# Performance work log

Measured on AMD Instinct MI355X. Metric: run time of the kernel, lower is better.

## Reference

```python
import jax, jax.numpy as jnp
from jax import lax
import numpy as np

L, T, B, F, H = 2, 512, 128, 4, 256


def _qweight(r, i, j, k):
    # Parcollet quaternion linear: W [in, out] from components [in//4, out//4]
    cr = jnp.concatenate([r, -i, -j, -k], axis=0)
    ci = jnp.concatenate([i, r, -k, j], axis=0)
    cj = jnp.concatenate([j, k, r, -i], axis=0)
    ck = jnp.concatenate([k, -j, i, r], axis=0)
    return jnp.concatenate([cr, ci, cj, ck], axis=1)


def _qlstm_layer(x, wr, wi, wj, wk, wb, ur, ui, uj, uk, fw, fb):
    # x: [T, B, F_in]; gate order (f, i, o, c) along axis 0 of the stacked params
    Wx = jax.vmap(_qweight)(wr, wi, wj, wk)          # [4, F_in, H]
    Uh = jax.vmap(_qweight)(ur, ui, uj, uk)          # [4, H, H]
    g = jnp.einsum('tbf,gfh->tgbh', x, Wx) + wb[None, :, None, :]  # [T,4,B,H]
    h0 = jnp.zeros((x.shape[1], Uh.shape[-1]), x.dtype)

    def step(carry, gt):
        h, c = carry
        pre = gt + jnp.einsum('bh,ghk->gbk', h, Uh)   # [4,B,H]
        ft = jax.nn.sigmoid(pre[0])
        it = jax.nn.sigmoid(pre[1])
        ot = jax.nn.sigmoid(pre[2])
        c = it * jnp.tanh(pre[3]) + ft * c
        h = ot * jnp.tanh(c)
        return (h, c), h @ fw + fb

    _, out = lax.scan(step, (h0, h0), g)              # [T, B, F_out]
    norm = jnp.linalg.norm(out, axis=2, keepdims=True)
    return out / jnp.maximum(norm, 1e-12)


def setup_inputs() -> dict:
    key = jax.random.key(0)
    ks = jax.random.split(key, 12)
    s = 0.05
    return {
        'x': jax.random.normal(ks[0], (B, T, F), jnp.float32),
        'Wx_r': jax.random.normal(ks[1], (L, 4, F // 4, H // 4), jnp.float32) * s,
        'Wx_i': jax.random.normal(ks[2], (L, 4, F // 4, H // 4), jnp.float32) * s,
        'Wx_j': jax.random.normal(ks[3], (L, 4, F // 4, H // 4), jnp.float32) * s,
        'Wx_k': jax.random.normal(ks[4], (L, 4, F // 4, H // 4), jnp.float32) * s,
        'Wx_b': jax.random.normal(ks[5], (L, 4, H), jnp.float32) * s,
        'Uh_r': jax.random.normal(ks[6], (L, 4, H // 4, H // 4), jnp.float32) * s,
        'Uh_i': jax.random.normal(ks[7], (L, 4, H // 4, H // 4), jnp.float32) * s,
        'Uh_j': jax.random.normal(ks[8], (L, 4, H // 4, H // 4), jnp.float32) * s,
        'Uh_k': jax.random.normal(ks[9], (L, 4, H // 4, H // 4), jnp.float32) * s,
        'fco_w': jax.random.normal(ks[10], (L, H, F), jnp.float32) * s,
        'fco_b': jax.random.normal(ks[11], (L, F), jnp.float32) * s,
    }


def reference(x, Wx_r, Wx_i, Wx_j, Wx_k, Wx_b, Uh_r, Uh_i, Uh_j, Uh_k, fco_w, fco_b):
    h = jnp.transpose(x, (1, 0, 2))  # batch_first -> [T, B, F]
    for l in range(L):
        h = _qlstm_layer(h, Wx_r[l], Wx_i[l], Wx_j[l], Wx_k[l], Wx_b[l],
                         Uh_r[l], Uh_i[l], Uh_j[l], Uh_k[l], fco_w[l], fco_b[l])
    h = jnp.transpose(h, (1, 0, 2))  # back to [B, T, F]
    return h[:, -1, :]
```

## Files before the change

kernel.cpp:

```cpp
#include <hip/hip_runtime.h>

#define L_ 2
#define T_ 512
#define B_ 128
#define F_ 4
#define H_ 256
#define QSIGN_MASK 0x5390
#define LOG2E  1.4426950408889634f
#define LOG2E2 2.8853900817779268f

typedef __attribute__((ext_vector_type(8))) short short8;
typedef __attribute__((ext_vector_type(4))) float f32x4;

__device__ unsigned long long g_inter_q[T_][B_];

__global__ void zero_inter() {
  ((unsigned long long*)g_inter_q)[blockIdx.x * 256 + threadIdx.x] = 0ull;
}

__device__ __forceinline__ unsigned f2bf(float f) {
  unsigned u = __float_as_uint(f);
  return (u + 0x7fff + ((u >> 16) & 1)) >> 16;
}
__device__ __forceinline__ float sig2(float y) {
  return __builtin_amdgcn_rcpf(1.f + __builtin_amdgcn_exp2f(-y));
}
__device__ __forceinline__ float tanh2(float y) {
  return fmaf(2.f, __builtin_amdgcn_rcpf(1.f + __builtin_amdgcn_exp2f(-y)), -1.f);
}
__device__ __forceinline__ unsigned long long pack4bf(float a, float b, float c, float d) {
  unsigned lo, hi;
  asm("v_cvt_pk_bf16_f32 %0, %1, %2" : "=v"(lo) : "v"(a), "v"(b));
  asm("v_cvt_pk_bf16_f32 %0, %1, %2" : "=v"(hi) : "v"(c), "v"(d));
  return ((unsigned long long)hi << 32) | lo;
}

union FragU { short8 v; uint4 u; unsigned w[4]; };

__launch_bounds__(320, 1)
__global__ void qlstm_fused(const float* __restrict__ x_in,
                            const float* __restrict__ uhr, const float* __restrict__ uhi,
                            const float* __restrict__ uhj, const float* __restrict__ uhk,
                            const float* __restrict__ wxr, const float* __restrict__ wxi,
                            const float* __restrict__ wxj, const float* __restrict__ wxk,
                            const float* __restrict__ wxb_all,
                            const float* __restrict__ fcw_all, const float* __restrict__ fcb_all,
                            float* __restrict__ out_final)
{
  __shared__ __align__(16) unsigned short sh_h[2][4][272];
  __shared__ unsigned long long sh_x[4][4];

  const int t     = threadIdx.x;
  const int role  = blockIdx.x >> 5;
  const int bg    = blockIdx.x & 31;
  const int bg0   = bg * 4;
  const int layer = role;
  const int wv    = t >> 6;
  const int lane  = t & 63;
  const int quad  = lane >> 4;
  const int sub   = lane & 15;

  const float* wb = wxb_all + layer * 4 * H_;
  const float* fw = fcw_all + layer * H_ * F_;
  const float* fb = fcb_all + layer * F_;

  for (int i = t; i < 2176; i += 320) ((unsigned short*)sh_h)[i] = 0;

  if (wv < 4) {
    const int u  = wv * 16 + sub;
    const int ba = sub >> 2;
    const int qa = sub & 3;

    FragU Bf[32];
    FragU Bx[4];
    f32x4 bvv[4];
    {
      const float* Cc[4] = {uhr, uhi, uhj, uhk};
      const float* Xc[4] = {wxr, wxi, wxj, wxk};
      #pragma unroll
      for (int g = 0; g < 4; ++g) {
        const float kg = (g == 3) ? LOG2E2 : LOG2E;
        #pragma unroll
        for (int ks = 0; ks < 8; ++ks) {
          const int d  = ks >> 1;
          const int pp = (ks & 1) * 32 + quad * 8;
          const float* src = Cc[d] + (size_t)((layer * 4 + g) * 64 + pp) * 64 + u;
          FragU f;
          #pragma unroll
          for (int j = 0; j < 8; ++j) f.v[j] = (short)f2bf(src[j * 64] * kg);
          Bf[g * 8 + ks] = f;
        }
        FragU fx; fx.w[0] = 0; fx.w[1] = 0; fx.w[2] = 0; fx.w[3] = 0;
        if (quad == 0) {
          unsigned e0 = f2bf(Xc[0][(layer * 4 + g) * 64 + u] * kg);
          unsigned e1 = f2bf(Xc[1][(layer * 4 + g) * 64 + u] * kg);
          unsigned e2 = f2bf(Xc[2][(layer * 4 + g) * 64 + u] * kg);
          unsigned e3 = f2bf(Xc[3][(layer * 4 + g) * 64 + u] * kg);
          fx.w[0] = e0 | (e1 << 16);
          fx.w[1] = e2 | (e3 << 16);
        }
        Bx[g] = fx;
        f32x4 bv;
        #pragma unroll
        for (int r = 0; r < 4; ++r) bv[r] = wb[g * 256 + r * 64 + u] * kg;
        bvv[g] = bv;
      }
    }
    unsigned smask[4], smx[4];
    int xsh[4], aoff[8];
    #pragma unroll
    for (int d = 0; d < 4; ++d) {
      const int a = qa ^ d;
      const bool neg = (QSIGN_MASK >> (a * 4 + qa)) & 1;
      smask[d] = neg ? 0x80008000u : 0u;
      smx[d]   = neg ? 0x8000u : 0u;
      xsh[d]   = 16 * a;
    }
    #pragma unroll
    for (int ks = 0; ks < 8; ++ks)
      aoff[ks] = ba * 544 + (((qa ^ (ks >> 1)) * 64 + (ks & 1) * 32 + quad * 8) << 1);
    float cs[4] = {0.f, 0.f, 0.f, 0.f};
    __syncthreads();

    const char* hbB = (const char*)sh_h;
    for (int s = 0; s <= T_; ++s) {
      if (s < T_) {
        const char* hp = hbB + ((s + 1) & 1) * 2176;
        unsigned long long xq = sh_x[s & 3][ba];
        FragU Ax; Ax.w[0] = 0; Ax.w[1] = 0; Ax.w[2] = 0; Ax.w[3] = 0;
        if (quad == 0) {
          unsigned e0 = ((unsigned)(xq >> xsh[0]) & 0xffffu) ^ smx[0];
          unsigned e1 = ((unsigned)(xq >> xsh[1]) & 0xffffu) ^ smx[1];
          unsigned e2 = ((unsigned)(xq >> xsh[2]) & 0xffffu) ^ smx[2];
          unsigned e3 = ((unsigned)(xq >> xsh[3]) & 0xffffu) ^ smx[3];
          Ax.w[0] = e0 | (e1 << 16);
          Ax.w[1] = e2 | (e3 << 16);
        }
        f32x4 acc0 = __builtin_amdgcn_mfma_f32_16x16x32_bf16(Ax.v, Bx[0].v, bvv[0], 0, 0, 0);
        f32x4 acc1 = __builtin_amdgcn_mfma_f32_16x16x32_bf16(Ax.v, Bx[1].v, bvv[1], 0, 0, 0);
        f32x4 acc2 = __builtin_amdgcn_mfma_f32_16x16x32_bf16(Ax.v, Bx[2].v, bvv[2], 0, 0, 0);
        f32x4 acc3 = __builtin_amdgcn_mfma_f32_16x16x32_bf16(Ax.v, Bx[3].v, bvv[3], 0, 0, 0);
        #pragma unroll
        for (int ks = 0; ks < 8; ++ks) {
          FragU A;
          A.u = *(const uint4*)(hp + aoff[ks]);
          const unsigned m = smask[ks >> 1];
          A.w[0] ^= m; A.w[1] ^= m; A.w[2] ^= m; A.w[3] ^= m;
          acc0 = __builtin_amdgcn_mfma_f32_16x16x32_bf16(A.v, Bf[0 * 8 + ks].v, acc0, 0, 0, 0);
          acc1 = __builtin_amdgcn_mfma_f32_16x16x32_bf16(A.v, Bf[1 * 8 + ks].v, acc1, 0, 0, 0);
          acc2 = __builtin_amdgcn_mfma_f32_16x16x32_bf16(A.v, Bf[2 * 8 + ks].v, acc2, 0, 0, 0);
          acc3 = __builtin_amdgcn_mfma_f32_16x16x32_bf16(A.v, Bf[3 * 8 + ks].v, acc3, 0, 0, 0);
        }
        float hv0, hv1, hv2, hv3;
        {
          float fg, ig, og, cv;
          fg = sig2(acc0[0]); ig = sig2(acc1[0]); og = sig2(acc2[0]); cv = tanh2(acc3[0]);
          cs[0] = ig * cv + fg * cs[0]; hv0 = og * tanh2(cs[0] * LOG2E2);
          fg = sig2(acc0[1]); ig = sig2(acc1[1]); og = sig2(acc2[1]); cv = tanh2(acc3[1]);
          cs[1] = ig * cv + fg * cs[1]; hv1 = og * tanh2(cs[1] * LOG2E2);
          fg = sig2(acc0[2]); ig = sig2(acc1[2]); og = sig2(acc2[2]); cv = tanh2(acc3[2]);
          cs[2] = ig * cv + fg * cs[2]; hv2 = og * tanh2(cs[2] * LOG2E2);
          fg = sig2(acc0[3]); ig = sig2(acc1[3]); og = sig2(acc2[3]); cv = tanh2(acc3[3]);
          cs[3] = ig * cv + fg * cs[3]; hv3 = og * tanh2(cs[3] * LOG2E2);
        }
        unsigned w01, w23;
        asm("v_cvt_pk_bf16_f32 %0, %1, %2" : "=v"(w01) : "v"(hv0), "v"(hv1));
        asm("v_cvt_pk_bf16_f32 %0, %1, %2" : "=v"(w23) : "v"(hv2), "v"(hv3));
        char* hw = (char*)sh_h + (s & 1) * 2176 + quad * 544;
        const int ub = u << 1;
        *(unsigned short*)(hw + ub)       = (unsigned short)w01;
        *(unsigned short*)(hw + 128 + ub) = (unsigned short)(w01 >> 16);
        *(unsigned short*)(hw + 256 + ub) = (unsigned short)w23;
        *(unsigned short*)(hw + 384 + ub) = (unsigned short)(w23 >> 16);
      }
      __syncthreads();
    }
  } else {
    FragU Af[8];
    #pragma unroll
    for (int ks = 0; ks < 8; ++ks) {
      FragU f;
      #pragma unroll
      for (int j = 0; j < 8; ++j) {
        const int k = ks * 32 + quad * 8 + j;
        f.v[j] = (sub < 4) ? (short)f2bf(fw[k * 4 + sub]) : (short)0;
      }
      Af[ks] = f;
    }
    const float fb0 = fb[0], fb1 = fb[1], fb2 = fb[2], fb3 = fb[3];
    const int bl = sub & 3;

    if (lane < 4) {
      #pragma unroll
      for (int s0 = 0; s0 < 2; ++s0) {
        if (role == 0) {
          float4 xv = *(const float4*)(x_in + (size_t)((bg0 + lane) * T_ + s0) * F_);
          sh_x[s0][lane] = pack4bf(xv.x, xv.y, xv.z, xv.w);
        } else {
          unsigned long long v;
          while ((v = __hip_atomic_load(&g_inter_q[s0][bg0 + lane], __ATOMIC_RELAXED,
                                        __HIP_MEMORY_SCOPE_AGENT)) == 0ull)
            __builtin_amdgcn_s_sleep(1);
          sh_x[s0][lane] = v;
        }
      }
    }
    unsigned long long heldq = 0ull;
    __syncthreads();

    for (int s = 0; s <= T_; ++s) {
      const bool doproj = (s >= 1) && (role == 0 || s == T_);
      if (doproj) {
        const char* hp = (const char*)sh_h + ((s + 1) & 1) * 2176;
        f32x4 pa = {fb0, fb1, fb2, fb3};
        #pragma unroll
        for (int ks = 0; ks < 8; ++ks) {
          FragU Bh;
          Bh.u = *(const uint4*)(hp + bl * 544 + ((ks * 32 + quad * 8) << 1));
          pa = __builtin_amdgcn_mfma_f32_16x16x32_bf16(Af[ks].v, Bh.v, pa, 0, 0, 0);
        }
        if (lane < 4) {
          float p0 = pa[0], p1 = pa[1], p2 = pa[2], p3 = pa[3];
          float inv = __builtin_amdgcn_rsqf(
              fmaxf(p0*p0 + p1*p1 + p2*p2 + p3*p3, 1e-24f));
          p0 *= inv; p1 *= inv; p2 *= inv; p3 *= inv;
          if (role == 0) {
            unsigned long long qw = pack4bf(p0, p1, p2, p3);
            if (s & 1) {
              heldq = qw;
            } else {
              __hip_atomic_store(&g_inter_q[s - 2][bg0 + lane], heldq,
                                 __ATOMIC_RELAXED, __HIP_MEMORY_SCOPE_AGENT);
              __hip_atomic_store(&g_inter_q[s - 1][bg0 + lane], qw,
                                 __ATOMIC_RELAXED, __HIP_MEMORY_SCOPE_AGENT);
            }
          } else {
            *(float4*)(out_final + (bg0 + lane) * F_) = make_float4(p0, p1, p2, p3);
          }
        }
      }
      if (lane < 4 && s + 2 < T_) {
        const int slot = (s + 2) & 3;
        if (role == 0) {
          float4 xv = *(const float4*)(x_in + (size_t)((bg0 + lane) * T_ + s + 2) * F_);
          sh_x[slot][lane] = pack4bf(xv.x, xv.y, xv.z, xv.w);
        } else {
          unsigned long long v;
          while ((v = __hip_atomic_load(&g_inter_q[s + 2][bg0 + lane], __ATOMIC_RELAXED,
                                        __HIP_MEMORY_SCOPE_AGENT)) == 0ull)
            __builtin_amdgcn_s_sleep(1);
          sh_x[slot][lane] = v;
        }
      }
      __syncthreads();
    }
  }
}

extern "C" void kernel_launch(void* const* d_in, const int* in_sizes, int n_in,
                              void* d_out, int out_size, void* d_ws, size_t ws_size,
                              hipStream_t stream) {
  const float* x   = (const float*)d_in[0];
  const float* wxr = (const float*)d_in[1];
  const float* wxi = (const float*)d_in[2];
  const float* wxj = (const float*)d_in[3];
  const float* wxk = (const float*)d_in[4];
  const float* wxb = (const float*)d_in[5];
  const float* uhr = (const float*)d_in[6];
  const float* uhi = (const float*)d_in[7];
  const float* uhj = (const float*)d_in[8];
  const float* uhk = (const float*)d_in[9];
  const float* fcw = (const float*)d_in[10];
  const float* fcb = (const float*)d_in[11];
  float* out = (float*)d_out;

  zero_inter<<<dim3(T_ * B_ / 256), dim3(256), 0, stream>>>();
  qlstm_fused<<<dim3(64), dim3(320), 0, stream>>>(
      x, uhr, uhi, uhj, uhk, wxr, wxi, wxj, wxk, wxb, fcw, fcb, out);
}
```

Measured before the change: 524.5 us.

## Store negated h copy in LDS, hoist global loads, use lighter barrier in helper wave

The recurrent waves now also write a sign-flipped copy of h into a second LDS plane, so the quaternion sign pattern is picked by address instead of XORing each A fragment per MFMA k-step. The helper wave issues its x / inter-layer global loads at the top of each step so they overlap the projection MFMAs. It stores each inter-layer value right away instead of batching pairs, and uses a barrier that waits only on LDS. This shortens the serial per-step critical path but doubles the h LDS writes and footprint.

```diff
diff --git a/kernel.cpp b/kernel.cpp
--- a/kernel.cpp
+++ b/kernel.cpp
@@ -36,6 +36,12 @@
 }
 
 union FragU { short8 v; uint4 u; unsigned w[4]; };
+
+#define HBAR() do { \
+  asm volatile("s_waitcnt lgkmcnt(0)" ::: "memory"); \
+  __builtin_amdgcn_s_barrier(); \
+  asm volatile("" ::: "memory"); \
+} while (0)
 
 __launch_bounds__(320, 1)
 __global__ void qlstm_fused(const float* __restrict__ x_in,
@@ -47,7 +53,7 @@
                             const float* __restrict__ fcw_all, const float* __restrict__ fcb_all,
                             float* __restrict__ out_final)
 {
-  __shared__ __align__(16) unsigned short sh_h[2][4][272];
+  __shared__ __align__(16) unsigned short sh_h[2][2][4][272];
   __shared__ unsigned long long sh_x[4][4];
 
   const int t     = threadIdx.x;
@@ -64,7 +70,7 @@
   const float* fw = fcw_all + layer * H_ * F_;
   const float* fb = fcb_all + layer * F_;
 
-  for (int i = t; i < 2176; i += 320) ((unsigned short*)sh_h)[i] = 0;
+  for (int i = t; i < 4352; i += 320) ((unsigned short*)sh_h)[i] = 0;
 
   if (wv < 4) {
     const int u  = wv * 16 + sub;
@@ -106,26 +112,30 @@
         bvv[g] = bv;
       }
     }
-    unsigned smask[4], smx[4];
+    unsigned smx[4];
     int xsh[4], aoff[8];
     #pragma unroll
     for (int d = 0; d < 4; ++d) {
       const int a = qa ^ d;
       const bool neg = (QSIGN_MASK >> (a * 4 + qa)) & 1;
-      smask[d] = neg ? 0x80008000u : 0u;
-      smx[d]   = neg ? 0x8000u : 0u;
-      xsh[d]   = 16 * a;
+      smx[d] = neg ? 0x8000u : 0u;
+      xsh[d] = 16 * a;
     }
     #pragma unroll
-    for (int ks = 0; ks < 8; ++ks)
-      aoff[ks] = ba * 544 + (((qa ^ (ks >> 1)) * 64 + (ks & 1) * 32 + quad * 8) << 1);
+    for (int ks = 0; ks < 8; ++ks) {
+      const int d = ks >> 1;
+      const int a = qa ^ d;
+      const bool neg = (QSIGN_MASK >> (a * 4 + qa)) & 1;
+      aoff[ks] = (neg ? 2176 : 0) + ba * 544
+               + ((a * 64 + (ks & 1) * 32 + quad * 8) << 1);
+    }
     float cs[4] = {0.f, 0.f, 0.f, 0.f};
     __syncthreads();
 
     const char* hbB = (const char*)sh_h;
     for (int s = 0; s <= T_; ++s) {
       if (s < T_) {
-        const char* hp = hbB + ((s + 1) & 1) * 2176;
+        const char* hp = hbB + ((s + 1) & 1) * 4352;
         unsigned long long xq = sh_x[s & 3][ba];
         FragU Ax; Ax.w[0] = 0; Ax.w[1] = 0; Ax.w[2] = 0; Ax.w[3] = 0;
         if (quad == 0) {
@@ -144,8 +154,6 @@
         for (int ks = 0; ks < 8; ++ks) {
           FragU A;
           A.u = *(const uint4*)(hp + aoff[ks]);
-          const unsigned m = smask[ks >> 1];
-          A.w[0] ^= m; A.w[1] ^= m; A.w[2] ^= m; A.w[3] ^= m;
           acc0 = __builtin_amdgcn_mfma_f32_16x16x32_bf16(A.v, Bf[0 * 8 + ks].v, acc0, 0, 0, 0);
           acc1 = __builtin_amdgcn_mfma_f32_16x16x32_bf16(A.v, Bf[1 * 8 + ks].v, acc1, 0, 0, 0);
           acc2 = __builtin_amdgcn_mfma_f32_16x16x32_bf16(A.v, Bf[2 * 8 + ks].v, acc2, 0, 0, 0);
@@ -166,12 +174,18 @@
         unsigned w01, w23;
         asm("v_cvt_pk_bf16_f32 %0, %1, %2" : "=v"(w01) : "v"(hv0), "v"(hv1));
         asm("v_cvt_pk_bf16_f32 %0, %1, %2" : "=v"(w23) : "v"(hv2), "v"(hv3));
-        char* hw = (char*)sh_h + (s & 1) * 2176 + quad * 544;
+        const unsigned n01 = w01 ^ 0x80008000u;
+        const unsigned n23 = w23 ^ 0x80008000u;
+        char* hw = (char*)sh_h + (s & 1) * 4352 + quad * 544;
         const int ub = u << 1;
-        *(unsigned short*)(hw + ub)       = (unsigned short)w01;
-        *(unsigned short*)(hw + 128 + ub) = (unsigned short)(w01 >> 16);
-        *(unsigned short*)(hw + 256 + ub) = (unsigned short)w23;
-        *(unsigned short*)(hw + 384 + ub) = (unsigned short)(w23 >> 16);
+        *(unsigned short*)(hw + ub)              = (unsigned short)w01;
+        *(unsigned short*)(hw + 128 + ub)        = (unsigned short)(w01 >> 16);
+        *(unsigned short*)(hw + 256 + ub)        = (unsigned short)w23;
+        *(unsigned short*)(hw + 384 + ub)        = (unsigned short)(w23 >> 16);
+        *(unsigned short*)(hw + 2176 + ub)       = (unsigned short)n01;
+        *(unsigned short*)(hw + 2176 + 128 + ub) = (unsigned short)(n01 >> 16);
+        *(unsigned short*)(hw + 2176 + 256 + ub) = (unsigned short)n23;
+        *(unsigned short*)(hw + 2176 + 384 + ub) = (unsigned short)(n23 >> 16);
       }
       __syncthreads();
     }
@@ -205,13 +219,22 @@
         }
       }
     }
-    unsigned long long heldq = 0ull;
-    __syncthreads();
+    HBAR();
 
     for (int s = 0; s <= T_; ++s) {
+      const bool stg = (lane < 4) && (s + 2 < T_);
+      float4 xv = make_float4(0.f, 0.f, 0.f, 0.f);
+      unsigned long long mv = 0ull;
+      if (stg) {
+        if (role == 0)
+          xv = *(const float4*)(x_in + (size_t)((bg0 + lane) * T_ + s + 2) * F_);
+        else
+          mv = __hip_atomic_load(&g_inter_q[s + 2][bg0 + lane], __ATOMIC_RELAXED,
+                                 __HIP_MEMORY_SCOPE_AGENT);
+      }
       const bool doproj = (s >= 1) && (role == 0 || s == T_);
       if (doproj) {
-        const char* hp = (const char*)sh_h + ((s + 1) & 1) * 2176;
+        const char* hp = (const char*)sh_h + ((s + 1) & 1) * 4352;
         f32x4 pa = {fb0, fb1, fb2, fb3};
         #pragma unroll
         for (int ks = 0; ks < 8; ++ks) {
@@ -225,34 +248,27 @@
               fmaxf(p0*p0 + p1*p1 + p2*p2 + p3*p3, 1e-24f));
           p0 *= inv; p1 *= inv; p2 *= inv; p3 *= inv;
           if (role == 0) {
-            unsigned long long qw = pack4bf(p0, p1, p2, p3);
-            if (s & 1) {
-              heldq = qw;
-            } else {
-              __hip_atomic_store(&g_inter_q[s - 2][bg0 + lane], heldq,
-                                 __ATOMIC_RELAXED, __HIP_MEMORY_SCOPE_AGENT);
-              __hip_atomic_store(&g_inter_q[s - 1][bg0 + lane], qw,
-                                 __ATOMIC_RELAXED, __HIP_MEMORY_SCOPE_AGENT);
-            }
+            __hip_atomic_store(&g_inter_q[s - 1][bg0 + lane], pack4bf(p0, p1, p2, p3),
+                               __ATOMIC_RELAXED, __HIP_MEMORY_SCOPE_AGENT);
           } else {
             *(float4*)(out_final + (bg0 + lane) * F_) = make_float4(p0, p1, p2, p3);
           }
         }
       }
-      if (lane < 4 && s + 2 < T_) {
+      if (stg) {
         const int slot = (s + 2) & 3;
         if (role == 0) {
-          float4 xv = *(const float4*)(x_in + (size_t)((bg0 + lane) * T_ + s + 2) * F_);
           sh_x[slot][lane] = pack4bf(xv.x, xv.y, xv.z, xv.w);
         } else {
-          unsigned long long v;
-          while ((v = __hip_atomic_load(&g_inter_q[s + 2][bg0 + lane], __ATOMIC_RELAXED,
-                                        __HIP_MEMORY_SCOPE_AGENT)) == 0ull)
+          while (mv == 0ull) {
             __builtin_amdgcn_s_sleep(1);
-          sh_x[slot][lane] = v;
-        }
-      }
-      __syncthreads();
+            mv = __hip_atomic_load(&g_inter_q[s + 2][bg0 + lane], __ATOMIC_RELAXED,
+                                   __HIP_MEMORY_SCOPE_AGENT);
+          }
+          sh_x[slot][lane] = mv;
+        }
+      }
+      HBAR();
     }
   }
 }
```

Measured after the change: 693.8 us. +32.3%, slower.
